# Performance work log

Hardware: AMD Instinct MI355X
Metric: run time of the kernel (lower is better)

The kernel has to match this reference:

```python
import jax, jax.numpy as jnp
import numpy as np

N, E, F_IN, HID, HEADS, B = 50000, 800000, 128, 128, 2, 256
EPS = 1e-5
NEG_SLOPE = 0.2


def gat_conv(x, src, dst, W, a_src, a_dst, b, heads, out_c, concat):
    n = x.shape[0]
    h = (x @ W).reshape(n, heads, out_c)            # [N,H,C]
    alpha_src = jnp.sum(h * a_src, axis=-1)          # [N,H]
    alpha_dst = jnp.sum(h * a_dst, axis=-1)          # [N,H]
    e = jax.nn.leaky_relu(alpha_src[src] + alpha_dst[dst], NEG_SLOPE)  # [E2,H]
    # segment softmax over incoming edges per destination node
    emax = jax.ops.segment_max(e, dst, num_segments=n)
    ex = jnp.exp(e - emax[dst])
    denom = jax.ops.segment_sum(ex, dst, num_segments=n)
    alpha = ex / denom[dst]                          # [E2,H]
    msg = h[src] * alpha[:, :, None]                 # [E2,H,C]
    out = jax.ops.segment_sum(msg, dst, num_segments=n)  # [N,H,C]
    if concat:
        out = out.reshape(n, heads * out_c)
    else:
        out = out.mean(axis=1)
    return out + b


def batchnorm_eval(x, gamma, beta, mean, var):
    return gamma * (x - mean) * jax.lax.rsqrt(var + EPS) + beta


def setup_inputs() -> dict:
    key = jax.random.key(0)
    ks = jax.random.split(key, 16)
    x = jax.random.normal(ks[0], (N, F_IN), dtype=jnp.float32)
    edge_index = jax.random.randint(ks[1], (2, E), 0, N, dtype=jnp.int64)
    batch = (jnp.arange(N, dtype=jnp.int64) * B) // N  # sorted, every graph non-empty
    s1 = 1.0 / np.sqrt(F_IN)
    s2 = 1.0 / np.sqrt(HEADS * HID)
    return {
        "x": x,
        "edge_index": edge_index,
        "batch": batch,
        "W1": jax.random.normal(ks[2], (F_IN, HEADS * HID), dtype=jnp.float32) * s1,
        "a_src1": jax.random.normal(ks[3], (HEADS, HID), dtype=jnp.float32) * s1,
        "a_dst1": jax.random.normal(ks[4], (HEADS, HID), dtype=jnp.float32) * s1,
        "b1": jnp.zeros((HEADS * HID,), dtype=jnp.float32),
        "gamma1": jnp.ones((HEADS * HID,), dtype=jnp.float32),
        "beta1": jnp.zeros((HEADS * HID,), dtype=jnp.float32),
        "rm1": jax.random.normal(ks[5], (HEADS * HID,), dtype=jnp.float32) * 0.1,
        "rv1": jax.random.uniform(ks[6], (HEADS * HID,), dtype=jnp.float32, minval=0.5, maxval=1.5),
        "W2": jax.random.normal(ks[7], (HEADS * HID, HID), dtype=jnp.float32) * s2,
        "a_src2": jax.random.normal(ks[8], (1, HID), dtype=jnp.float32) * s2,
        "a_dst2": jax.random.normal(ks[9], (1, HID), dtype=jnp.float32) * s2,
        "b2": jnp.zeros((HID,), dtype=jnp.float32),
        "gamma2": jnp.ones((HID,), dtype=jnp.float32),
        "beta2": jnp.zeros((HID,), dtype=jnp.float32),
        "rm2": jax.random.normal(ks[10], (HID,), dtype=jnp.float32) * 0.1,
        "rv2": jax.random.uniform(ks[11], (HID,), dtype=jnp.float32, minval=0.5, maxval=1.5),
    }


def reference(x, edge_index, batch, W1, a_src1, a_dst1, b1, gamma1, beta1, rm1, rv1,
              W2, a_src2, a_dst2, b2, gamma2, beta2, rm2, rv2):
    n = x.shape[0]
    # PyG GATConv adds self-loops by default
    loops = jnp.arange(n, dtype=edge_index.dtype)
    src = jnp.concatenate([edge_index[0], loops])
    dst = jnp.concatenate([edge_index[1], loops])

    h = gat_conv(x, src, dst, W1, a_src1, a_dst1, b1, HEADS, HID, concat=True)
    h = jax.nn.relu(batchnorm_eval(h, gamma1, beta1, rm1, rv1))  # dropout = identity (eval)

    h = gat_conv(h, src, dst, W2, a_src2, a_dst2, b2, 1, HID, concat=False)
    h = jax.nn.relu(batchnorm_eval(h, gamma2, beta2, rm2, rv2))

    # global max pool over graphs
    h_D = jax.ops.segment_max(h, batch, num_segments=B)  # [B, HID]
    return h_D
```

## Files before the change

### kernel.cpp

```cpp
#include <hip/hip_runtime.h>
#include <hip/hip_bf16.h>
#include <math.h>

#define NEG_SLOPE 0.2f
#define EPSBN 1e-5f

typedef __attribute__((ext_vector_type(8))) short bf16x8;
typedef __attribute__((ext_vector_type(4))) float f32x4;

__device__ __forceinline__ float bfu2f(unsigned u_lo16) { return __uint_as_float(u_lo16 << 16); }
__device__ __forceinline__ unsigned short f2bf(float f) {
    return __bfloat16_as_ushort(__float2bfloat16(f));
}
__device__ __forceinline__ void splitf(float v, unsigned short &h, unsigned short &l) {
    __hip_bfloat16 hb = __float2bfloat16(v);
    float r = v - __bfloat162float(hb);
    h = __bfloat16_as_ushort(hb);
    l = __bfloat16_as_ushort(__float2bfloat16(r));
}

__global__ void split_x4(const float* __restrict__ X, unsigned short* __restrict__ Xh,
                         unsigned short* __restrict__ Xl, int total4)
{
    int i = blockIdx.x * blockDim.x + threadIdx.x;
    if (i >= total4) return;
    float4 v = *(const float4*)(X + (size_t)i * 4);
    unsigned short h[4], l[4];
    splitf(v.x, h[0], l[0]); splitf(v.y, h[1], l[1]);
    splitf(v.z, h[2], l[2]); splitf(v.w, h[3], l[3]);
    *(uint2*)(Xh + (size_t)i * 4) = *(uint2*)h;
    *(uint2*)(Xl + (size_t)i * 4) = *(uint2*)l;
}

__global__ void split_w_both(const float* __restrict__ W1, const float* __restrict__ W2,
                             unsigned short* __restrict__ w1th, unsigned short* __restrict__ w1tl,
                             unsigned short* __restrict__ w2th, unsigned short* __restrict__ w2tl)
{
    int idx = blockIdx.x * blockDim.x + threadIdx.x;
    if (idx < 32768) {
        int nn = idx >> 7, k = idx & 127;
        unsigned short h, l; splitf(W1[(size_t)k * 256 + nn], h, l);
        w1th[idx] = h; w1tl[idx] = l;
    } else if (idx < 65536) {
        int j = idx - 32768;
        int nn = j >> 8, k = j & 255;
        unsigned short h, l; splitf(W2[(size_t)k * 128 + nn], h, l);
        w2th[j] = h; w2tl[j] = l;
    }
}

__global__ __launch_bounds__(256) void gemm_bf16_split_attn(
    const unsigned short* __restrict__ Ah, const unsigned short* __restrict__ Al,
    const unsigned short* __restrict__ Bth, const unsigned short* __restrict__ Btl,
    unsigned short* __restrict__ Cb,
    const float* __restrict__ aSrc, const float* __restrict__ aDst,
    float* __restrict__ asrcOut, float* __restrict__ adstOut,
    int M, int N, int K, int heads)
{
    __shared__ unsigned short smem[4][128][32];
    const int tid = threadIdx.x;
    const int lane = tid & 63;
    const int wave = tid >> 6;
    const int fr = lane & 15, g = lane >> 4;
    const int wr = (wave >> 1) * 64, wc = (wave & 1) * 64;
    const int rowBase = blockIdx.x * 128, colBase = blockIdx.y * 128;

    f32x4 acc[4][4] = {};

    for (int kk = 0; kk < K; kk += 32) {
#pragma unroll
        for (int i = 0; i < 2; ++i) {
            int idx = tid + 256 * i;
            int r = idx >> 2, c = (idx & 3) * 8;
            int grow = rowBase + r;
            uint4 va_h, va_l;
            if (grow < M) {
                va_h = *(const uint4*)(Ah + (size_t)grow * K + kk + c);
                va_l = *(const uint4*)(Al + (size_t)grow * K + kk + c);
            } else {
                va_h = make_uint4(0, 0, 0, 0); va_l = make_uint4(0, 0, 0, 0);
            }
            *(uint4*)&smem[0][r][c] = va_h;
            *(uint4*)&smem[1][r][c] = va_l;
            int gcol = colBase + r;
            *(uint4*)&smem[2][r][c] = *(const uint4*)(Bth + (size_t)gcol * K + kk + c);
            *(uint4*)&smem[3][r][c] = *(const uint4*)(Btl + (size_t)gcol * K + kk + c);
        }
        __syncthreads();

        bf16x8 ah[4], al[4], bh[4], bl[4];
#pragma unroll
        for (int m = 0; m < 4; ++m) {
            ah[m] = *(const bf16x8*)&smem[0][wr + m * 16 + fr][g * 8];
            al[m] = *(const bf16x8*)&smem[1][wr + m * 16 + fr][g * 8];
        }
#pragma unroll
        for (int n = 0; n < 4; ++n) {
            bh[n] = *(const bf16x8*)&smem[2][wc + n * 16 + fr][g * 8];
            bl[n] = *(const bf16x8*)&smem[3][wc + n * 16 + fr][g * 8];
        }
#pragma unroll
        for (int m = 0; m < 4; ++m)
#pragma unroll
            for (int n = 0; n < 4; ++n) {
                acc[m][n] = __builtin_amdgcn_mfma_f32_16x16x32_bf16(ah[m], bh[n], acc[m][n], 0, 0, 0);
                acc[m][n] = __builtin_amdgcn_mfma_f32_16x16x32_bf16(ah[m], bl[n], acc[m][n], 0, 0, 0);
                acc[m][n] = __builtin_amdgcn_mfma_f32_16x16x32_bf16(al[m], bh[n], acc[m][n], 0, 0, 0);
            }
        __syncthreads();
    }

    {
        const int head = colBase >> 7;
        float avs[4], avd[4];
#pragma unroll
        for (int n = 0; n < 4; ++n) {
            int col = colBase + wc + n * 16 + fr;
            avs[n] = aSrc[col]; avd[n] = aDst[col];
        }
#pragma unroll
        for (int m = 0; m < 4; ++m) {
            float ps[4], pd[4];
#pragma unroll
            for (int j = 0; j < 4; ++j) {
                ps[j] = acc[m][0][j] * avs[0] + acc[m][1][j] * avs[1]
                      + acc[m][2][j] * avs[2] + acc[m][3][j] * avs[3];
                pd[j] = acc[m][0][j] * avd[0] + acc[m][1][j] * avd[1]
                      + acc[m][2][j] * avd[2] + acc[m][3][j] * avd[3];
            }
#pragma unroll
            for (int off = 8; off; off >>= 1)
#pragma unroll
                for (int j = 0; j < 4; ++j) {
                    ps[j] += __shfl_xor(ps[j], off);
                    pd[j] += __shfl_xor(pd[j], off);
                }
            if (fr == 0) {
#pragma unroll
                for (int j = 0; j < 4; ++j) {
                    int grow = rowBase + wr + m * 16 + g * 4 + j;
                    if (grow < M) {
                        atomicAdd(asrcOut + (size_t)grow * heads + head, ps[j]);
                        atomicAdd(adstOut + (size_t)grow * heads + head, pd[j]);
                    }
                }
            }
        }
    }

    float* Cs = (float*)&smem[0][0][0];
    const int rl_w = (wr >> 6) * 16;
#pragma unroll
    for (int m = 0; m < 4; ++m) {
        __syncthreads();
#pragma unroll
        for (int n = 0; n < 4; ++n)
#pragma unroll
            for (int j = 0; j < 4; ++j)
                Cs[(rl_w + g * 4 + j) * 132 + wc + n * 16 + fr] = acc[m][n][j];
        __syncthreads();
        int rl = tid >> 3, c16 = (tid & 7) * 16;
        int grow = rowBase + (rl >> 4) * 64 + m * 16 + (rl & 15);
        if (grow < M) {
            unsigned short tmp[16];
#pragma unroll
            for (int i = 0; i < 16; ++i) tmp[i] = f2bf(Cs[rl * 132 + c16 + i]);
            *(uint4*)(Cb + (size_t)grow * N + colBase + c16)     = *(uint4*)&tmp[0];
            *(uint4*)(Cb + (size_t)grow * N + colBase + c16 + 8) = *(uint4*)&tmp[8];
        }
    }
}

__global__ void count_edges(const int* __restrict__ ei, int E, int Nn,
                            int* __restrict__ counts, int* __restrict__ erank)
{
    int e = blockIdx.x * blockDim.x + threadIdx.x;
    int E2 = E + Nn;
    if (e >= E2) return;
    int dst = (e < E) ? ei[E + e] : (e - E);
    erank[e] = atomicAdd(&counts[dst], 1);
}

__global__ __launch_bounds__(256) void scan_block(
    const int* __restrict__ counts, int* __restrict__ offs, int* __restrict__ bsum, int Nn)
{
    __shared__ int s[256];
    int i = blockIdx.x * 256 + threadIdx.x;
    int v = (i < Nn) ? counts[i] : 0;
    s[threadIdx.x] = v;
    __syncthreads();
    for (int off = 1; off < 256; off <<= 1) {
        int t = (threadIdx.x >= off) ? s[threadIdx.x - off] : 0;
        __syncthreads();
        s[threadIdx.x] += t;
        __syncthreads();
    }
    if (i < Nn) offs[i] = s[threadIdx.x] - v;
    if (threadIdx.x == 255) bsum[blockIdx.x] = s[255];
}

__global__ __launch_bounds__(256) void scan_tops(int* __restrict__ bsum, int* __restrict__ boff, int nb)
{
    __shared__ int s[256];
    int v = (threadIdx.x < nb) ? bsum[threadIdx.x] : 0;
    s[threadIdx.x] = v;
    __syncthreads();
    for (int off = 1; off < 256; off <<= 1) {
        int t = (threadIdx.x >= off) ? s[threadIdx.x - off] : 0;
        __syncthreads();
        s[threadIdx.x] += t;
        __syncthreads();
    }
    if (threadIdx.x < nb) boff[threadIdx.x] = s[threadIdx.x] - v;
}

__global__ void add_offsets(int* __restrict__ offs, const int* __restrict__ boff, int Nn, int E2)
{
    int i = blockIdx.x * blockDim.x + threadIdx.x;
    if (i < Nn) offs[i] += boff[i >> 8];
    if (i == 0) offs[Nn] = E2;
}

__global__ void fill_edges(const int* __restrict__ ei, int E, int Nn,
                           const int* __restrict__ offs, const int* __restrict__ erank,
                           int* __restrict__ esrc)
{
    int e = blockIdx.x * blockDim.x + threadIdx.x;
    int E2 = E + Nn;
    if (e >= E2) return;
    int src, dst;
    if (e < E) { src = ei[e]; dst = ei[E + e]; }
    else       { src = e - E; dst = e - E; }
    esrc[offs[dst] + erank[e]] = src;
}

__device__ __forceinline__ void fma8(float wA, uint4 hv, float acc[8])
{
    acc[0] = fmaf(wA, bfu2f(hv.x & 0xffff), acc[0]);
    acc[1] = fmaf(wA, __uint_as_float(hv.x & 0xffff0000u), acc[1]);
    acc[2] = fmaf(wA, bfu2f(hv.y & 0xffff), acc[2]);
    acc[3] = fmaf(wA, __uint_as_float(hv.y & 0xffff0000u), acc[3]);
    acc[4] = fmaf(wA, bfu2f(hv.z & 0xffff), acc[4]);
    acc[5] = fmaf(wA, __uint_as_float(hv.z & 0xffff0000u), acc[5]);
    acc[6] = fmaf(wA, bfu2f(hv.w & 0xffff), acc[6]);
    acc[7] = fmaf(wA, __uint_as_float(hv.w & 0xffff0000u), acc[7]);
}

__device__ __forceinline__ void gather2h(
    int sj, float w0, float w1, int nc, int sub, int head,
    const char* __restrict__ hb_c, float acc[8])
{
    int t = 0;
    for (; t + 8 <= nc; t += 8) {
        int e0 = t + sub;
        int sA0 = __shfl(sj, e0),     sA1 = __shfl(sj, e0 + 2);
        int sA2 = __shfl(sj, e0 + 4), sA3 = __shfl(sj, e0 + 6);
        float a0 = __shfl(w0, e0),     a1 = __shfl(w0, e0 + 2);
        float a2 = __shfl(w0, e0 + 4), a3 = __shfl(w0, e0 + 6);
        float b0 = __shfl(w1, e0),     b1 = __shfl(w1, e0 + 2);
        float b2 = __shfl(w1, e0 + 4), b3 = __shfl(w1, e0 + 6);
        uint4 h0 = *(const uint4*)(hb_c + sA0 * 512);
        uint4 h1 = *(const uint4*)(hb_c + sA1 * 512);
        uint4 h2 = *(const uint4*)(hb_c + sA2 * 512);
        uint4 h3 = *(const uint4*)(hb_c + sA3 * 512);
        fma8(head ? b0 : a0, h0, acc);
        fma8(head ? b1 : a1, h1, acc);
        fma8(head ? b2 : a2, h2, acc);
        fma8(head ? b3 : a3, h3, acc);
    }
    for (; t < nc; t += 2) {
        int e = t + sub;
        int sA = __shfl(sj, e);
        float a = __shfl(w0, e), b = __shfl(w1, e);
        uint4 hv = *(const uint4*)(hb_c + sA * 512);
        fma8(head ? b : a, hv, acc);
    }
}

__device__ __forceinline__ void gather1h(
    int sj, float w, int nc, int sub,
    const char* __restrict__ hb_c, float acc[8])
{
    int t = 0;
    for (; t + 16 <= nc; t += 16) {
        int e0 = t + sub;
        int sA0 = __shfl(sj, e0),     sA1 = __shfl(sj, e0 + 4);
        int sA2 = __shfl(sj, e0 + 8), sA3 = __shfl(sj, e0 + 12);
        float w0 = __shfl(w, e0),     w1 = __shfl(w, e0 + 4);
        float w2 = __shfl(w, e0 + 8), w3 = __shfl(w, e0 + 12);
        uint4 h0 = *(const uint4*)(hb_c + sA0 * 256);
        uint4 h1 = *(const uint4*)(hb_c + sA1 * 256);
        uint4 h2 = *(const uint4*)(hb_c + sA2 * 256);
        uint4 h3 = *(const uint4*)(hb_c + sA3 * 256);
        fma8(w0, h0, acc);
        fma8(w1, h1, acc);
        fma8(w2, h2, acc);
        fma8(w3, h3, acc);
    }
    for (; t < nc; t += 4) {
        int e = t + sub;
        int sA = __shfl(sj, e);
        float wA = __shfl(w, e);
        uint4 hv = *(const uint4*)(hb_c + sA * 256);
        fma8(wA, hv, acc);
    }
}

__global__ __launch_bounds__(256) void spmm1(
    const unsigned short* __restrict__ h1b, const float* __restrict__ asrc,
    const float* __restrict__ adst, const int* __restrict__ offs,
    const int* __restrict__ esrc,
    const float* __restrict__ b1, const float* __restrict__ gamma,
    const float* __restrict__ beta, const float* __restrict__ rm,
    const float* __restrict__ rv, unsigned short* __restrict__ x2h,
    unsigned short* __restrict__ x2l, int Nn)
{
    int d = (int)((blockIdx.x * blockDim.x + threadIdx.x) >> 6);
    int lane = threadIdx.x & 63;
    if (d >= Nn) return;
    int beg = offs[d], end = offs[d + 1];
    int deg = end - beg;
    float ad0 = adst[d * 2], ad1 = adst[d * 2 + 1];
    const int sub = lane >> 5;
    const int cgrp = lane & 31;
    const int head = cgrp >> 4;
    const char* hb_c = (const char*)h1b + cgrp * 16;
    float acc[8] = {};

    if (deg <= 64) {
        int sj = 0; float e0 = -1e30f, e1 = -1e30f;
        if (lane < deg) {
            sj = esrc[beg + lane];
            float2 av = *(const float2*)(asrc + (size_t)sj * 2);
            e0 = av.x + ad0; e0 = e0 > 0.f ? e0 : NEG_SLOPE * e0;
            e1 = av.y + ad1; e1 = e1 > 0.f ? e1 : NEG_SLOPE * e1;
        }
        float m0 = e0, m1 = e1;
        for (int off = 32; off; off >>= 1) {
            m0 = fmaxf(m0, __shfl_xor(m0, off));
            m1 = fmaxf(m1, __shfl_xor(m1, off));
        }
        float p0 = (lane < deg) ? expf(e0 - m0) : 0.f;
        float p1 = (lane < deg) ? expf(e1 - m1) : 0.f;
        float s0 = p0, s1 = p1;
        for (int off = 32; off; off >>= 1) {
            s0 += __shfl_xor(s0, off);
            s1 += __shfl_xor(s1, off);
        }
        float w0 = p0 * (1.f / s0), w1 = p1 * (1.f / s1);
        gather2h(sj, w0, w1, deg, sub, head, hb_c, acc);
    } else {
        float m0 = -1e30f, m1 = -1e30f;
        for (int j = beg + lane; j < end; j += 64) {
            int s = esrc[j];
            float2 av = *(const float2*)(asrc + (size_t)s * 2);
            float e0 = av.x + ad0; e0 = e0 > 0.f ? e0 : NEG_SLOPE * e0;
            float e1 = av.y + ad1; e1 = e1 > 0.f ? e1 : NEG_SLOPE * e1;
            m0 = fmaxf(m0, e0); m1 = fmaxf(m1, e1);
        }
        for (int off = 32; off; off >>= 1) {
            m0 = fmaxf(m0, __shfl_xor(m0, off));
            m1 = fmaxf(m1, __shfl_xor(m1, off));
        }
        float s0 = 0.f, s1 = 0.f;
        for (int j = beg + lane; j < end; j += 64) {
            int s = esrc[j];
            float2 av = *(const float2*)(asrc + (size_t)s * 2);
            float e0 = av.x + ad0; e0 = e0 > 0.f ? e0 : NEG_SLOPE * e0;
            float e1 = av.y + ad1; e1 = e1 > 0.f ? e1 : NEG_SLOPE * e1;
            s0 += expf(e0 - m0); s1 += expf(e1 - m1);
        }
        for (int off = 32; off; off >>= 1) {
            s0 += __shfl_xor(s0, off);
            s1 += __shfl_xor(s1, off);
        }
        float rd0 = 1.f / s0, rd1 = 1.f / s1;
        for (int base = beg; base < end; base += 64) {
            int nc = end - base; if (nc > 64) nc = 64;
            int sj = 0; float w0 = 0.f, w1 = 0.f;
            if (lane < nc) {
                sj = esrc[base + lane];
                float2 av = *(const float2*)(asrc + (size_t)sj * 2);
                float e0 = av.x + ad0; e0 = e0 > 0.f ? e0 : NEG_SLOPE * e0;
                float e1 = av.y + ad1; e1 = e1 > 0.f ? e1 : NEG_SLOPE * e1;
                w0 = expf(e0 - m0) * rd0;
                w1 = expf(e1 - m1) * rd1;
            }
            gather2h(sj, w0, w1, nc, sub, head, hb_c, acc);
        }
    }
#pragma unroll
    for (int i = 0; i < 8; ++i) acc[i] += __shfl_xor(acc[i], 32);
    if (lane < 32) {
        int cl = cgrp * 8;
        unsigned short hh[8], ll[8];
#pragma unroll
        for (int i = 0; i < 8; ++i) {
            int c = cl + i;
            float v = acc[i] + b1[c];
            v = gamma[c] * (v - rm[c]) * rsqrtf(rv[c] + EPSBN) + beta[c];
            v = fmaxf(v, 0.f);
            splitf(v, hh[i], ll[i]);
        }
        *(uint4*)(x2h + (size_t)d * 256 + cl) = *(uint4*)&hh[0];
        *(uint4*)(x2l + (size_t)d * 256 + cl) = *(uint4*)&ll[0];
    }
}

__global__ __launch_bounds__(256) void spmm2(
    const unsigned short* __restrict__ h2b, const float* __restrict__ asrc,
    const float* __restrict__ adst, const int* __restrict__ offs,
    const int* __restrict__ esrc,
    const float* __restrict__ b2, const float* __restrict__ gamma,
    const float* __restrict__ beta, const float* __restrict__ rm,
    const float* __restrict__ rv, float* __restrict__ x3, int Nn)
{
    int d = (int)((blockIdx.x * blockDim.x + threadIdx.x) >> 6);
    int lane = threadIdx.x & 63;
    if (d >= Nn) return;
    int beg = offs[d], end = offs[d + 1];
    int deg = end - beg;
    float ad = adst[d];
    const int sub = lane >> 4;
    const int cgrp = lane & 15;
    const char* hb_c = (const char*)h2b + cgrp * 16;
    float acc[8] = {};

    if (deg <= 64) {
        int sj = 0; float ev = -1e30f;
        if (lane < deg) {
            sj = esrc[beg + lane];
            float e = asrc[sj] + ad; ev = e > 0.f ? e : NEG_SLOPE * e;
        }
        float m = ev;
        for (int off = 32; off; off >>= 1) m = fmaxf(m, __shfl_xor(m, off));
        float p = (lane < deg) ? expf(ev - m) : 0.f;
        float s = p;
        for (int off = 32; off; off >>= 1) s += __shfl_xor(s, off);
        float w = p * (1.f / s);
        gather1h(sj, w, deg, sub, hb_c, acc);
    } else {
        float m = -1e30f;
        for (int j = beg + lane; j < end; j += 64) {
            int s = esrc[j];
            float e = asrc[s] + ad; e = e > 0.f ? e : NEG_SLOPE * e;
            m = fmaxf(m, e);
        }
        for (int off = 32; off; off >>= 1) m = fmaxf(m, __shfl_xor(m, off));
        float sd = 0.f;
        for (int j = beg + lane; j < end; j += 64) {
            int s = esrc[j];
            float e = asrc[s] + ad; e = e > 0.f ? e : NEG_SLOPE * e;
            sd += expf(e - m);
        }
        for (int off = 32; off; off >>= 1) sd += __shfl_xor(sd, off);
        float rd = 1.f / sd;
        for (int base = beg; base < end; base += 64) {
            int nc = end - base; if (nc > 64) nc = 64;
            int sj = 0; float wj = 0.f;
            if (lane < nc) {
                sj = esrc[base + lane];
                float e = asrc[sj] + ad; e = e > 0.f ? e : NEG_SLOPE * e;
                wj = expf(e - m) * rd;
            }
            gather1h(sj, wj, nc, sub, hb_c, acc);
        }
    }
#pragma unroll
    for (int i = 0; i < 8; ++i) {
        acc[i] += __shfl_xor(acc[i], 32);
        acc[i] += __shfl_xor(acc[i], 16);
    }
    if (lane < 16) {
        int cl = cgrp * 8;
        float vv[8];
#pragma unroll
        for (int i = 0; i < 8; ++i) {
            int c = cl + i;
            float v = acc[i] + b2[c];
            v = gamma[c] * (v - rm[c]) * rsqrtf(rv[c] + EPSBN) + beta[c];
            vv[i] = fmaxf(v, 0.f);
        }
        *(float4*)(x3 + (size_t)d * 128 + cl)     = make_float4(vv[0], vv[1], vv[2], vv[3]);
        *(float4*)(x3 + (size_t)d * 128 + cl + 4) = make_float4(vv[4], vv[5], vv[6], vv[7]);
    }
}

__global__ __launch_bounds__(128) void pool_max_graph(
    const float* __restrict__ x3, const int* __restrict__ bat,
    float* __restrict__ out, int Nn)
{
    int g = blockIdx.x;
    int c = threadIdx.x;
    int lo = 0, hi = Nn;
    while (lo < hi) { int mid = (lo + hi) >> 1; if (bat[mid] < g) lo = mid + 1; else hi = mid; }
    int beg = lo;
    hi = Nn;
    while (lo < hi) { int mid = (lo + hi) >> 1; if (bat[mid] < g + 1) lo = mid + 1; else hi = mid; }
    int end = lo;
    float acc = -1e30f;
    for (int n = beg; n < end; ++n)
        acc = fmaxf(acc, x3[(size_t)n * 128 + c]);
    out[(size_t)g * 128 + c] = acc;
}

extern "C" void kernel_launch(void* const* d_in, const int* in_sizes, int n_in,
                              void* d_out, int out_size, void* d_ws, size_t ws_size,
                              hipStream_t stream)
{
    const float* x   = (const float*)d_in[0];
    const int*   ei  = (const int*)d_in[1];
    const int*   bat = (const int*)d_in[2];
    const float* W1  = (const float*)d_in[3];
    const float* as1 = (const float*)d_in[4];
    const float* ad1 = (const float*)d_in[5];
    const float* b1  = (const float*)d_in[6];
    const float* g1  = (const float*)d_in[7];
    const float* be1 = (const float*)d_in[8];
    const float* rm1 = (const float*)d_in[9];
    const float* rv1 = (const float*)d_in[10];
    const float* W2  = (const float*)d_in[11];
    const float* as2 = (const float*)d_in[12];
    const float* ad2 = (const float*)d_in[13];
    const float* b2  = (const float*)d_in[14];
    const float* g2  = (const float*)d_in[15];
    const float* be2 = (const float*)d_in[16];
    const float* rm2 = (const float*)d_in[17];
    const float* rv2 = (const float*)d_in[18];
    float* out = (float*)d_out;

    const int Nn = in_sizes[0] / 128;
    const int E  = in_sizes[1] / 2;
    const int E2 = E + Nn;
    const int B  = out_size / 128;

    char* p = (char*)d_ws;
    size_t off = 0;
    auto alloc = [&](size_t bytes) -> void* {
        void* r = p + off;
        off = (off + bytes + 255) & ~(size_t)255;
        return r;
    };
    unsigned short* xh    = (unsigned short*)alloc((size_t)Nn * 128 * 2);
    unsigned short* xl    = (unsigned short*)alloc((size_t)Nn * 128 * 2);
    unsigned short* w1th  = (unsigned short*)alloc(256 * 128 * 2);
    unsigned short* w1tl  = (unsigned short*)alloc(256 * 128 * 2);
    unsigned short* w2th  = (unsigned short*)alloc(128 * 256 * 2);
    unsigned short* w2tl  = (unsigned short*)alloc(128 * 256 * 2);
    unsigned short* h1b   = (unsigned short*)alloc((size_t)Nn * 256 * 2);
    unsigned short* x2h   = (unsigned short*)alloc((size_t)Nn * 256 * 2);
    unsigned short* x2l   = (unsigned short*)alloc((size_t)Nn * 256 * 2);
    unsigned short* h2b   = (unsigned short*)alloc((size_t)Nn * 128 * 2);
    float*          x3    = (float*)alloc((size_t)Nn * 128 * 4);
    float*          attnv = (float*)alloc((size_t)Nn * 6 * 4);
    float*          asrc1 = attnv;
    float*          adst1 = attnv + (size_t)Nn * 2;
    float*          asrc2 = attnv + (size_t)Nn * 4;
    float*          adst2 = attnv + (size_t)Nn * 5;
    int*            counts= (int*)alloc((size_t)Nn * 4);
    int*            erank = (int*)alloc((size_t)E2 * 4);
    int*            offs  = (int*)alloc((size_t)(Nn + 1) * 4);
    int*            bsum  = (int*)alloc(256 * 4);
    int*            boff  = (int*)alloc(256 * 4);
    int*            esrc  = (int*)alloc((size_t)E2 * 4);

    const int nb = (Nn + 255) / 256;
    const int nwB = (Nn + 3) / 4;
    const int gmB = (Nn + 127) / 128;

    hipMemsetAsync(counts, 0, (size_t)Nn * 4, stream);
    hipMemsetAsync(attnv, 0, (size_t)Nn * 6 * 4, stream);

    split_x4<<<(Nn * 128 / 4 + 255) / 256, 256, 0, stream>>>(x, xh, xl, Nn * 128 / 4);
    split_w_both<<<(65536 + 255) / 256, 256, 0, stream>>>(W1, W2, w1th, w1tl, w2th, w2tl);

    count_edges<<<(E2 + 255) / 256, 256, 0, stream>>>(ei, E, Nn, counts, erank);
    scan_block<<<nb, 256, 0, stream>>>(counts, offs, bsum, Nn);
    scan_tops<<<1, 256, 0, stream>>>(bsum, boff, nb);
    add_offsets<<<(Nn + 255) / 256, 256, 0, stream>>>(offs, boff, Nn, E2);
    fill_edges<<<(E2 + 255) / 256, 256, 0, stream>>>(ei, E, Nn, offs, erank, esrc);

    gemm_bf16_split_attn<<<dim3(gmB, 2), 256, 0, stream>>>(
        xh, xl, w1th, w1tl, h1b, as1, ad1, asrc1, adst1, Nn, 256, 128, 2);
    spmm1<<<nwB, 256, 0, stream>>>(h1b, asrc1, adst1, offs, esrc,
                                   b1, g1, be1, rm1, rv1, x2h, x2l, Nn);

    gemm_bf16_split_attn<<<dim3(gmB, 1), 256, 0, stream>>>(
        x2h, x2l, w2th, w2tl, h2b, as2, ad2, asrc2, adst2, Nn, 128, 256, 1);
    spmm2<<<nwB, 256, 0, stream>>>(h2b, asrc2, adst2, offs, esrc,
                                   b2, g2, be2, rm2, rv2, x3, Nn);

    pool_max_graph<<<B, 128, 0, stream>>>(x3, bat, out, Nn);
}
```

Baseline: 281.3 us.

## Reorder layer-1 GAT to aggregate raw features before the weight GEMM

Layer-1 attention logits are now computed directly from x using precomputed vectors W1·a_src and W1·a_dst, fused into the input split kernel. The sparse aggregation then gathers 128-wide raw input rows (256 B bf16) per edge instead of 256-wide projected rows, producing a per-head aggregated input [N,256]. A new GEMM applies each head's W1 slice and fuses bias, batchnorm and ReLU into its epilogue. This halves the gather traffic per edge in exchange for writing and re-reading a larger split-precision intermediate. Layer-1 aggregation also loses precision, since it now sums bf16-rounded x (high part only) where the old path summed bf16 h.

```diff
diff --git a/kernel.cpp b/kernel.cpp
--- a/kernel.cpp
+++ b/kernel.cpp
@@ -19,17 +19,48 @@
     l = __bfloat16_as_ushort(__float2bfloat16(r));
 }
 
-__global__ void split_x4(const float* __restrict__ X, unsigned short* __restrict__ Xh,
-                         unsigned short* __restrict__ Xl, int total4)
-{
-    int i = blockIdx.x * blockDim.x + threadIdx.x;
-    if (i >= total4) return;
-    float4 v = *(const float4*)(X + (size_t)i * 4);
-    unsigned short h[4], l[4];
-    splitf(v.x, h[0], l[0]); splitf(v.y, h[1], l[1]);
-    splitf(v.z, h[2], l[2]); splitf(v.w, h[3], l[3]);
-    *(uint2*)(Xh + (size_t)i * 4) = *(uint2*)h;
-    *(uint2*)(Xl + (size_t)i * 4) = *(uint2*)l;
+__global__ void precompute_v(const float* __restrict__ W1, const float* __restrict__ as1,
+                             const float* __restrict__ ad1, float* __restrict__ vsd)
+{
+    int k = threadIdx.x;
+    if (k >= 128) return;
+    float v0 = 0.f, v1 = 0.f, v2 = 0.f, v3 = 0.f;
+    const float* wr = W1 + (size_t)k * 256;
+    for (int c = 0; c < 128; ++c) {
+        float wa = wr[c], wb = wr[128 + c];
+        v0 += wa * as1[c];  v1 += wb * as1[128 + c];
+        v2 += wa * ad1[c];  v3 += wb * ad1[128 + c];
+    }
+    vsd[k] = v0; vsd[128 + k] = v1; vsd[256 + k] = v2; vsd[384 + k] = v3;
+}
+
+__global__ __launch_bounds__(256) void split_x_attn(
+    const float* __restrict__ X, const float* __restrict__ vsd,
+    unsigned short* __restrict__ Xh, unsigned short* __restrict__ Xl,
+    float* __restrict__ asrc, float* __restrict__ adst, int Nn)
+{
+    int n = (int)((blockIdx.x * blockDim.x + threadIdx.x) >> 6);
+    int lane = threadIdx.x & 63;
+    if (n >= Nn) return;
+    float2 xv = *(const float2*)(X + (size_t)n * 128 + lane * 2);
+    unsigned short h0, l0, h1, l1;
+    splitf(xv.x, h0, l0); splitf(xv.y, h1, l1);
+    unsigned short hh[2] = {h0, h1}, ll[2] = {l0, l1};
+    *(unsigned*)(Xh + (size_t)n * 128 + lane * 2) = *(unsigned*)hh;
+    *(unsigned*)(Xl + (size_t)n * 128 + lane * 2) = *(unsigned*)ll;
+    int k = lane * 2;
+    float p0 = xv.x * vsd[k]       + xv.y * vsd[k + 1];
+    float p1 = xv.x * vsd[128 + k] + xv.y * vsd[129 + k];
+    float p2 = xv.x * vsd[256 + k] + xv.y * vsd[257 + k];
+    float p3 = xv.x * vsd[384 + k] + xv.y * vsd[385 + k];
+    for (int off = 32; off; off >>= 1) {
+        p0 += __shfl_xor(p0, off); p1 += __shfl_xor(p1, off);
+        p2 += __shfl_xor(p2, off); p3 += __shfl_xor(p3, off);
+    }
+    if (lane == 0) {
+        asrc[n * 2] = p0; asrc[n * 2 + 1] = p1;
+        adst[n * 2] = p2; adst[n * 2 + 1] = p3;
+    }
 }
 
 __global__ void split_w_both(const float* __restrict__ W1, const float* __restrict__ W2,
@@ -46,6 +77,329 @@
         int nn = j >> 8, k = j & 255;
         unsigned short h, l; splitf(W2[(size_t)k * 128 + nn], h, l);
         w2th[j] = h; w2tl[j] = l;
+    }
+}
+
+__global__ void count_edges(const int* __restrict__ ei, int E, int Nn,
+                            int* __restrict__ counts, int* __restrict__ erank)
+{
+    int e = blockIdx.x * blockDim.x + threadIdx.x;
+    int E2 = E + Nn;
+    if (e >= E2) return;
+    int dst = (e < E) ? ei[E + e] : (e - E);
+    erank[e] = atomicAdd(&counts[dst], 1);
+}
+
+__global__ __launch_bounds__(256) void scan_block(
+    const int* __restrict__ counts, int* __restrict__ offs, int* __restrict__ bsum, int Nn)
+{
+    __shared__ int s[256];
+    int i = blockIdx.x * 256 + threadIdx.x;
+    int v = (i < Nn) ? counts[i] : 0;
+    s[threadIdx.x] = v;
+    __syncthreads();
+    for (int off = 1; off < 256; off <<= 1) {
+        int t = (threadIdx.x >= off) ? s[threadIdx.x - off] : 0;
+        __syncthreads();
+        s[threadIdx.x] += t;
+        __syncthreads();
+    }
+    if (i < Nn) offs[i] = s[threadIdx.x] - v;
+    if (threadIdx.x == 255) bsum[blockIdx.x] = s[255];
+}
+
+__global__ __launch_bounds__(256) void scan_tops(int* __restrict__ bsum, int* __restrict__ boff, int nb)
+{
+    __shared__ int s[256];
+    int v = (threadIdx.x < nb) ? bsum[threadIdx.x] : 0;
+    s[threadIdx.x] = v;
+    __syncthreads();
+    for (int off = 1; off < 256; off <<= 1) {
+        int t = (threadIdx.x >= off) ? s[threadIdx.x - off] : 0;
+        __syncthreads();
+        s[threadIdx.x] += t;
+        __syncthreads();
+    }
+    if (threadIdx.x < nb) boff[threadIdx.x] = s[threadIdx.x] - v;
+}
+
+__global__ void add_offsets(int* __restrict__ offs, const int* __restrict__ boff, int Nn, int E2)
+{
+    int i = blockIdx.x * blockDim.x + threadIdx.x;
+    if (i < Nn) offs[i] += boff[i >> 8];
+    if (i == 0) offs[Nn] = E2;
+}
+
+__global__ void fill_edges(const int* __restrict__ ei, int E, int Nn,
+                           const int* __restrict__ offs, const int* __restrict__ erank,
+                           int* __restrict__ esrc)
+{
+    int e = blockIdx.x * blockDim.x + threadIdx.x;
+    int E2 = E + Nn;
+    if (e >= E2) return;
+    int src, dst;
+    if (e < E) { src = ei[e]; dst = ei[E + e]; }
+    else       { src = e - E; dst = e - E; }
+    esrc[offs[dst] + erank[e]] = src;
+}
+
+__device__ __forceinline__ void fma8(float wA, uint4 hv, float acc[8])
+{
+    acc[0] = fmaf(wA, bfu2f(hv.x & 0xffff), acc[0]);
+    acc[1] = fmaf(wA, __uint_as_float(hv.x & 0xffff0000u), acc[1]);
+    acc[2] = fmaf(wA, bfu2f(hv.y & 0xffff), acc[2]);
+    acc[3] = fmaf(wA, __uint_as_float(hv.y & 0xffff0000u), acc[3]);
+    acc[4] = fmaf(wA, bfu2f(hv.z & 0xffff), acc[4]);
+    acc[5] = fmaf(wA, __uint_as_float(hv.z & 0xffff0000u), acc[5]);
+    acc[6] = fmaf(wA, bfu2f(hv.w & 0xffff), acc[6]);
+    acc[7] = fmaf(wA, __uint_as_float(hv.w & 0xffff0000u), acc[7]);
+}
+
+__device__ __forceinline__ void fma8x2(float wa, float wb, uint4 hv,
+                                       float a0[8], float a1[8])
+{
+    float f;
+    f = bfu2f(hv.x & 0xffff);                 a0[0]=fmaf(wa,f,a0[0]); a1[0]=fmaf(wb,f,a1[0]);
+    f = __uint_as_float(hv.x & 0xffff0000u);  a0[1]=fmaf(wa,f,a0[1]); a1[1]=fmaf(wb,f,a1[1]);
+    f = bfu2f(hv.y & 0xffff);                 a0[2]=fmaf(wa,f,a0[2]); a1[2]=fmaf(wb,f,a1[2]);
+    f = __uint_as_float(hv.y & 0xffff0000u);  a0[3]=fmaf(wa,f,a0[3]); a1[3]=fmaf(wb,f,a1[3]);
+    f = bfu2f(hv.z & 0xffff);                 a0[4]=fmaf(wa,f,a0[4]); a1[4]=fmaf(wb,f,a1[4]);
+    f = __uint_as_float(hv.z & 0xffff0000u);  a0[5]=fmaf(wa,f,a0[5]); a1[5]=fmaf(wb,f,a1[5]);
+    f = bfu2f(hv.w & 0xffff);                 a0[6]=fmaf(wa,f,a0[6]); a1[6]=fmaf(wb,f,a1[6]);
+    f = __uint_as_float(hv.w & 0xffff0000u);  a0[7]=fmaf(wa,f,a0[7]); a1[7]=fmaf(wb,f,a1[7]);
+}
+
+__device__ __forceinline__ void gather1h(
+    int sj, float w, int nc, int sub,
+    const char* __restrict__ hb_c, float acc[8])
+{
+    for (int t = 0; t < nc; t += 4) {
+        int e = t + sub;
+        int sA = __shfl(sj, e);
+        float wA = __shfl(w, e);
+        uint4 hv = *(const uint4*)(hb_c + sA * 256);
+        fma8(wA, hv, acc);
+    }
+}
+
+__device__ __forceinline__ void gatherx(
+    int sj, float w0, float w1, int nc, int sub,
+    const char* __restrict__ hb_c, float a0[8], float a1[8])
+{
+    for (int t = 0; t < nc; t += 4) {
+        int e = t + sub;
+        int sA = __shfl(sj, e);
+        float wa = __shfl(w0, e);
+        float wb = __shfl(w1, e);
+        uint4 hv = *(const uint4*)(hb_c + sA * 256);
+        fma8x2(wa, wb, hv, a0, a1);
+    }
+}
+
+__global__ __launch_bounds__(256) void spmm_x(
+    const unsigned short* __restrict__ xh, const float* __restrict__ asrc,
+    const float* __restrict__ adst, const int* __restrict__ offs,
+    const int* __restrict__ esrc,
+    unsigned short* __restrict__ xth, unsigned short* __restrict__ xtl, int Nn)
+{
+    int d = (int)((blockIdx.x * blockDim.x + threadIdx.x) >> 6);
+    int lane = threadIdx.x & 63;
+    if (d >= Nn) return;
+    int beg = offs[d], end = offs[d + 1];
+    int deg = end - beg;
+    float ad0 = adst[d * 2], ad1 = adst[d * 2 + 1];
+    const int sub = lane >> 4;
+    const int cgrp = lane & 15;
+    const char* hb_c = (const char*)xh + cgrp * 16;
+    float a0[8] = {}, a1[8] = {};
+
+    if (deg <= 64) {
+        int sj = 0; float e0 = -1e30f, e1 = -1e30f;
+        if (lane < deg) {
+            sj = esrc[beg + lane];
+            float2 av = *(const float2*)(asrc + (size_t)sj * 2);
+            e0 = av.x + ad0; e0 = e0 > 0.f ? e0 : NEG_SLOPE * e0;
+            e1 = av.y + ad1; e1 = e1 > 0.f ? e1 : NEG_SLOPE * e1;
+        }
+        float m0 = e0, m1 = e1;
+        for (int off = 32; off; off >>= 1) {
+            m0 = fmaxf(m0, __shfl_xor(m0, off));
+            m1 = fmaxf(m1, __shfl_xor(m1, off));
+        }
+        float p0 = (lane < deg) ? expf(e0 - m0) : 0.f;
+        float p1 = (lane < deg) ? expf(e1 - m1) : 0.f;
+        float s0 = p0, s1 = p1;
+        for (int off = 32; off; off >>= 1) {
+            s0 += __shfl_xor(s0, off);
+            s1 += __shfl_xor(s1, off);
+        }
+        float w0 = p0 * (1.f / s0), w1 = p1 * (1.f / s1);
+        gatherx(sj, w0, w1, deg, sub, hb_c, a0, a1);
+    } else {
+        float m0 = -1e30f, m1 = -1e30f;
+        for (int j = beg + lane; j < end; j += 64) {
+            int s = esrc[j];
+            float2 av = *(const float2*)(asrc + (size_t)s * 2);
+            float e0 = av.x + ad0; e0 = e0 > 0.f ? e0 : NEG_SLOPE * e0;
+            float e1 = av.y + ad1; e1 = e1 > 0.f ? e1 : NEG_SLOPE * e1;
+            m0 = fmaxf(m0, e0); m1 = fmaxf(m1, e1);
+        }
+        for (int off = 32; off; off >>= 1) {
+            m0 = fmaxf(m0, __shfl_xor(m0, off));
+            m1 = fmaxf(m1, __shfl_xor(m1, off));
+        }
+        float s0 = 0.f, s1 = 0.f;
+        for (int j = beg + lane; j < end; j += 64) {
+            int s = esrc[j];
+            float2 av = *(const float2*)(asrc + (size_t)s * 2);
+            float e0 = av.x + ad0; e0 = e0 > 0.f ? e0 : NEG_SLOPE * e0;
+            float e1 = av.y + ad1; e1 = e1 > 0.f ? e1 : NEG_SLOPE * e1;
+            s0 += expf(e0 - m0); s1 += expf(e1 - m1);
+        }
+        for (int off = 32; off; off >>= 1) {
+            s0 += __shfl_xor(s0, off);
+            s1 += __shfl_xor(s1, off);
+        }
+        float rd0 = 1.f / s0, rd1 = 1.f / s1;
+        for (int base = beg; base < end; base += 64) {
+            int nc = end - base; if (nc > 64) nc = 64;
+            int sj = 0; float w0 = 0.f, w1 = 0.f;
+            if (lane < nc) {
+                sj = esrc[base + lane];
+                float2 av = *(const float2*)(asrc + (size_t)sj * 2);
+                float e0 = av.x + ad0; e0 = e0 > 0.f ? e0 : NEG_SLOPE * e0;
+                float e1 = av.y + ad1; e1 = e1 > 0.f ? e1 : NEG_SLOPE * e1;
+                w0 = expf(e0 - m0) * rd0;
+                w1 = expf(e1 - m1) * rd1;
+            }
+            gatherx(sj, w0, w1, nc, sub, hb_c, a0, a1);
+        }
+    }
+#pragma unroll
+    for (int i = 0; i < 8; ++i) {
+        a0[i] += __shfl_xor(a0[i], 32); a0[i] += __shfl_xor(a0[i], 16);
+        a1[i] += __shfl_xor(a1[i], 32); a1[i] += __shfl_xor(a1[i], 16);
+    }
+    if (lane < 16) {
+        int cl = cgrp * 8;
+        unsigned short h0[8], l0[8], h1[8], l1[8];
+#pragma unroll
+        for (int i = 0; i < 8; ++i) {
+            splitf(a0[i], h0[i], l0[i]);
+            splitf(a1[i], h1[i], l1[i]);
+        }
+        size_t rb = (size_t)d * 256;
+        *(uint4*)(xth + rb + cl)       = *(uint4*)&h0[0];
+        *(uint4*)(xtl + rb + cl)       = *(uint4*)&l0[0];
+        *(uint4*)(xth + rb + 128 + cl) = *(uint4*)&h1[0];
+        *(uint4*)(xtl + rb + 128 + cl) = *(uint4*)&l1[0];
+    }
+}
+
+__global__ __launch_bounds__(256) void gemm_bn_split(
+    const unsigned short* __restrict__ Ah, const unsigned short* __restrict__ Al,
+    const unsigned short* __restrict__ Bth, const unsigned short* __restrict__ Btl,
+    const float* __restrict__ bias, const float* __restrict__ gamma,
+    const float* __restrict__ beta, const float* __restrict__ rm,
+    const float* __restrict__ rv,
+    unsigned short* __restrict__ Ch, unsigned short* __restrict__ Cl, int M)
+{
+    __shared__ unsigned short smem[4][128][32];
+    const int tid = threadIdx.x;
+    const int lane = tid & 63;
+    const int wave = tid >> 6;
+    const int fr = lane & 15, g = lane >> 4;
+    const int wr = (wave >> 1) * 64, wc = (wave & 1) * 64;
+    const int rowBase = blockIdx.x * 128, colBase = blockIdx.y * 128;
+
+    f32x4 acc[4][4] = {};
+
+    for (int kk = 0; kk < 128; kk += 32) {
+#pragma unroll
+        for (int i = 0; i < 2; ++i) {
+            int idx = tid + 256 * i;
+            int r = idx >> 2, c = (idx & 3) * 8;
+            int grow = rowBase + r;
+            uint4 va_h, va_l;
+            if (grow < M) {
+                va_h = *(const uint4*)(Ah + (size_t)grow * 256 + colBase + kk + c);
+                va_l = *(const uint4*)(Al + (size_t)grow * 256 + colBase + kk + c);
+            } else {
+                va_h = make_uint4(0, 0, 0, 0); va_l = make_uint4(0, 0, 0, 0);
+            }
+            *(uint4*)&smem[0][r][c] = va_h;
+            *(uint4*)&smem[1][r][c] = va_l;
+            int gcol = colBase + r;
+            *(uint4*)&smem[2][r][c] = *(const uint4*)(Bth + (size_t)gcol * 128 + kk + c);
+            *(uint4*)&smem[3][r][c] = *(const uint4*)(Btl + (size_t)gcol * 128 + kk + c);
+        }
+        __syncthreads();
+
+        bf16x8 ah[4], al[4], bh[4], bl[4];
+#pragma unroll
+        for (int m = 0; m < 4; ++m) {
+            ah[m] = *(const bf16x8*)&smem[0][wr + m * 16 + fr][g * 8];
+            al[m] = *(const bf16x8*)&smem[1][wr + m * 16 + fr][g * 8];
+        }
+#pragma unroll
+        for (int n = 0; n < 4; ++n) {
+            bh[n] = *(const bf16x8*)&smem[2][wc + n * 16 + fr][g * 8];
+            bl[n] = *(const bf16x8*)&smem[3][wc + n * 16 + fr][g * 8];
+        }
+#pragma unroll
+        for (int m = 0; m < 4; ++m)
+#pragma unroll
+            for (int n = 0; n < 4; ++n) {
+                acc[m][n] = __builtin_amdgcn_mfma_f32_16x16x32_bf16(ah[m], bh[n], acc[m][n], 0, 0, 0);
+                acc[m][n] = __builtin_amdgcn_mfma_f32_16x16x32_bf16(ah[m], bl[n], acc[m][n], 0, 0, 0);
+                acc[m][n] = __builtin_amdgcn_mfma_f32_16x16x32_bf16(al[m], bh[n], acc[m][n], 0, 0, 0);
+            }
+        __syncthreads();
+    }
+
+    {
+        float bi[4], ga[4], bb[4], mu[4], iv[4];
+#pragma unroll
+        for (int n = 0; n < 4; ++n) {
+            int c = colBase + wc + n * 16 + fr;
+            bi[n] = bias[c]; ga[n] = gamma[c]; bb[n] = beta[c];
+            mu[n] = rm[c];   iv[n] = rsqrtf(rv[c] + EPSBN);
+        }
+#pragma unroll
+        for (int m = 0; m < 4; ++m)
+#pragma unroll
+            for (int n = 0; n < 4; ++n)
+#pragma unroll
+                for (int j = 0; j < 4; ++j) {
+                    float v = acc[m][n][j] + bi[n];
+                    v = ga[n] * (v - mu[n]) * iv[n] + bb[n];
+                    acc[m][n][j] = fmaxf(v, 0.f);
+                }
+    }
+
+    float* Cs = (float*)&smem[0][0][0];
+    const int rl_w = (wr >> 6) * 16;
+#pragma unroll
+    for (int m = 0; m < 4; ++m) {
+        __syncthreads();
+#pragma unroll
+        for (int n = 0; n < 4; ++n)
+#pragma unroll
+            for (int j = 0; j < 4; ++j)
+                Cs[(rl_w + g * 4 + j) * 132 + wc + n * 16 + fr] = acc[m][n][j];
+        __syncthreads();
+        int rl = tid >> 3, c16 = (tid & 7) * 16;
+        int grow = rowBase + (rl >> 4) * 64 + m * 16 + (rl & 15);
+        if (grow < M) {
+            unsigned short th[16], tl[16];
+#pragma unroll
+            for (int i = 0; i < 16; ++i) splitf(Cs[rl * 132 + c16 + i], th[i], tl[i]);
+            size_t ob = (size_t)grow * 256 + colBase + c16;
+            *(uint4*)(Ch + ob)     = *(uint4*)&th[0];
+            *(uint4*)(Ch + ob + 8) = *(uint4*)&th[8];
+            *(uint4*)(Cl + ob)     = *(uint4*)&tl[0];
+            *(uint4*)(Cl + ob + 8) = *(uint4*)&tl[8];
+        }
     }
 }
 
@@ -168,242 +522,6 @@
             *(uint4*)(Cb + (size_t)grow * N + colBase + c16)     = *(uint4*)&tmp[0];
             *(uint4*)(Cb + (size_t)grow * N + colBase + c16 + 8) = *(uint4*)&tmp[8];
         }
-    }
-}
-
-__global__ void count_edges(const int* __restrict__ ei, int E, int Nn,
-                            int* __restrict__ counts, int* __restrict__ erank)
-{
-    int e = blockIdx.x * blockDim.x + threadIdx.x;
-    int E2 = E + Nn;
-    if (e >= E2) return;
-    int dst = (e < E) ? ei[E + e] : (e - E);
-    erank[e] = atomicAdd(&counts[dst], 1);
-}
-
-__global__ __launch_bounds__(256) void scan_block(
-    const int* __restrict__ counts, int* __restrict__ offs, int* __restrict__ bsum, int Nn)
-{
-    __shared__ int s[256];
-    int i = blockIdx.x * 256 + threadIdx.x;
-    int v = (i < Nn) ? counts[i] : 0;
-    s[threadIdx.x] = v;
-    __syncthreads();
-    for (int off = 1; off < 256; off <<= 1) {
-        int t = (threadIdx.x >= off) ? s[threadIdx.x - off] : 0;
-        __syncthreads();
-        s[threadIdx.x] += t;
-        __syncthreads();
-    }
-    if (i < Nn) offs[i] = s[threadIdx.x] - v;
-    if (threadIdx.x == 255) bsum[blockIdx.x] = s[255];
-}
-
-__global__ __launch_bounds__(256) void scan_tops(int* __restrict__ bsum, int* __restrict__ boff, int nb)
-{
-    __shared__ int s[256];
-    int v = (threadIdx.x < nb) ? bsum[threadIdx.x] : 0;
-    s[threadIdx.x] = v;
-    __syncthreads();
-    for (int off = 1; off < 256; off <<= 1) {
-        int t = (threadIdx.x >= off) ? s[threadIdx.x - off] : 0;
-        __syncthreads();
-        s[threadIdx.x] += t;
-        __syncthreads();
-    }
-    if (threadIdx.x < nb) boff[threadIdx.x] = s[threadIdx.x] - v;
-}
-
-__global__ void add_offsets(int* __restrict__ offs, const int* __restrict__ boff, int Nn, int E2)
-{
-    int i = blockIdx.x * blockDim.x + threadIdx.x;
-    if (i < Nn) offs[i] += boff[i >> 8];
-    if (i == 0) offs[Nn] = E2;
-}
-
-__global__ void fill_edges(const int* __restrict__ ei, int E, int Nn,
-                           const int* __restrict__ offs, const int* __restrict__ erank,
-                           int* __restrict__ esrc)
-{
-    int e = blockIdx.x * blockDim.x + threadIdx.x;
-    int E2 = E + Nn;
-    if (e >= E2) return;
-    int src, dst;
-    if (e < E) { src = ei[e]; dst = ei[E + e]; }
-    else       { src = e - E; dst = e - E; }
-    esrc[offs[dst] + erank[e]] = src;
-}
-
-__device__ __forceinline__ void fma8(float wA, uint4 hv, float acc[8])
-{
-    acc[0] = fmaf(wA, bfu2f(hv.x & 0xffff), acc[0]);
-    acc[1] = fmaf(wA, __uint_as_float(hv.x & 0xffff0000u), acc[1]);
-    acc[2] = fmaf(wA, bfu2f(hv.y & 0xffff), acc[2]);
-    acc[3] = fmaf(wA, __uint_as_float(hv.y & 0xffff0000u), acc[3]);
-    acc[4] = fmaf(wA, bfu2f(hv.z & 0xffff), acc[4]);
-    acc[5] = fmaf(wA, __uint_as_float(hv.z & 0xffff0000u), acc[5]);
-    acc[6] = fmaf(wA, bfu2f(hv.w & 0xffff), acc[6]);
-    acc[7] = fmaf(wA, __uint_as_float(hv.w & 0xffff0000u), acc[7]);
-}
-
-__device__ __forceinline__ void gather2h(
-    int sj, float w0, float w1, int nc, int sub, int head,
-    const char* __restrict__ hb_c, float acc[8])
-{
-    int t = 0;
-    for (; t + 8 <= nc; t += 8) {
-        int e0 = t + sub;
-        int sA0 = __shfl(sj, e0),     sA1 = __shfl(sj, e0 + 2);
-        int sA2 = __shfl(sj, e0 + 4), sA3 = __shfl(sj, e0 + 6);
-        float a0 = __shfl(w0, e0),     a1 = __shfl(w0, e0 + 2);
-        float a2 = __shfl(w0, e0 + 4), a3 = __shfl(w0, e0 + 6);
-        float b0 = __shfl(w1, e0),     b1 = __shfl(w1, e0 + 2);
-        float b2 = __shfl(w1, e0 + 4), b3 = __shfl(w1, e0 + 6);
-        uint4 h0 = *(const uint4*)(hb_c + sA0 * 512);
-        uint4 h1 = *(const uint4*)(hb_c + sA1 * 512);
-        uint4 h2 = *(const uint4*)(hb_c + sA2 * 512);
-        uint4 h3 = *(const uint4*)(hb_c + sA3 * 512);
-        fma8(head ? b0 : a0, h0, acc);
-        fma8(head ? b1 : a1, h1, acc);
-        fma8(head ? b2 : a2, h2, acc);
-        fma8(head ? b3 : a3, h3, acc);
-    }
-    for (; t < nc; t += 2) {
-        int e = t + sub;
-        int sA = __shfl(sj, e);
-        float a = __shfl(w0, e), b = __shfl(w1, e);
-        uint4 hv = *(const uint4*)(hb_c + sA * 512);
-        fma8(head ? b : a, hv, acc);
-    }
-}
-
-__device__ __forceinline__ void gather1h(
-    int sj, float w, int nc, int sub,
-    const char* __restrict__ hb_c, float acc[8])
-{
-    int t = 0;
-    for (; t + 16 <= nc; t += 16) {
-        int e0 = t + sub;
-        int sA0 = __shfl(sj, e0),     sA1 = __shfl(sj, e0 + 4);
-        int sA2 = __shfl(sj, e0 + 8), sA3 = __shfl(sj, e0 + 12);
-        float w0 = __shfl(w, e0),     w1 = __shfl(w, e0 + 4);
-        float w2 = __shfl(w, e0 + 8), w3 = __shfl(w, e0 + 12);
-        uint4 h0 = *(const uint4*)(hb_c + sA0 * 256);
-        uint4 h1 = *(const uint4*)(hb_c + sA1 * 256);
-        uint4 h2 = *(const uint4*)(hb_c + sA2 * 256);
-        uint4 h3 = *(const uint4*)(hb_c + sA3 * 256);
-        fma8(w0, h0, acc);
-        fma8(w1, h1, acc);
-        fma8(w2, h2, acc);
-        fma8(w3, h3, acc);
-    }
-    for (; t < nc; t += 4) {
-        int e = t + sub;
-        int sA = __shfl(sj, e);
-        float wA = __shfl(w, e);
-        uint4 hv = *(const uint4*)(hb_c + sA * 256);
-        fma8(wA, hv, acc);
-    }
-}
-
-__global__ __launch_bounds__(256) void spmm1(
-    const unsigned short* __restrict__ h1b, const float* __restrict__ asrc,
-    const float* __restrict__ adst, const int* __restrict__ offs,
-    const int* __restrict__ esrc,
-    const float* __restrict__ b1, const float* __restrict__ gamma,
-    const float* __restrict__ beta, const float* __restrict__ rm,
-    const float* __restrict__ rv, unsigned short* __restrict__ x2h,
-    unsigned short* __restrict__ x2l, int Nn)
-{
-    int d = (int)((blockIdx.x * blockDim.x + threadIdx.x) >> 6);
-    int lane = threadIdx.x & 63;
-    if (d >= Nn) return;
-    int beg = offs[d], end = offs[d + 1];
-    int deg = end - beg;
-    float ad0 = adst[d * 2], ad1 = adst[d * 2 + 1];
-    const int sub = lane >> 5;
-    const int cgrp = lane & 31;
-    const int head = cgrp >> 4;
-    const char* hb_c = (const char*)h1b + cgrp * 16;
-    float acc[8] = {};
-
-    if (deg <= 64) {
-        int sj = 0; float e0 = -1e30f, e1 = -1e30f;
-        if (lane < deg) {
-            sj = esrc[beg + lane];
-            float2 av = *(const float2*)(asrc + (size_t)sj * 2);
-            e0 = av.x + ad0; e0 = e0 > 0.f ? e0 : NEG_SLOPE * e0;
-            e1 = av.y + ad1; e1 = e1 > 0.f ? e1 : NEG_SLOPE * e1;
-        }
-        float m0 = e0, m1 = e1;
-        for (int off = 32; off; off >>= 1) {
-            m0 = fmaxf(m0, __shfl_xor(m0, off));
-            m1 = fmaxf(m1, __shfl_xor(m1, off));
-        }
-        float p0 = (lane < deg) ? expf(e0 - m0) : 0.f;
-        float p1 = (lane < deg) ? expf(e1 - m1) : 0.f;
-        float s0 = p0, s1 = p1;
-        for (int off = 32; off; off >>= 1) {
-            s0 += __shfl_xor(s0, off);
-            s1 += __shfl_xor(s1, off);
-        }
-        float w0 = p0 * (1.f / s0), w1 = p1 * (1.f / s1);
-        gather2h(sj, w0, w1, deg, sub, head, hb_c, acc);
-    } else {
-        float m0 = -1e30f, m1 = -1e30f;
-        for (int j = beg + lane; j < end; j += 64) {
-            int s = esrc[j];
-            float2 av = *(const float2*)(asrc + (size_t)s * 2);
-            float e0 = av.x + ad0; e0 = e0 > 0.f ? e0 : NEG_SLOPE * e0;
-            float e1 = av.y + ad1; e1 = e1 > 0.f ? e1 : NEG_SLOPE * e1;
-            m0 = fmaxf(m0, e0); m1 = fmaxf(m1, e1);
-        }
-        for (int off = 32; off; off >>= 1) {
-            m0 = fmaxf(m0, __shfl_xor(m0, off));
-            m1 = fmaxf(m1, __shfl_xor(m1, off));
-        }
-        float s0 = 0.f, s1 = 0.f;
-        for (int j = beg + lane; j < end; j += 64) {
-            int s = esrc[j];
-            float2 av = *(const float2*)(asrc + (size_t)s * 2);
-            float e0 = av.x + ad0; e0 = e0 > 0.f ? e0 : NEG_SLOPE * e0;
-            float e1 = av.y + ad1; e1 = e1 > 0.f ? e1 : NEG_SLOPE * e1;
-            s0 += expf(e0 - m0); s1 += expf(e1 - m1);
-        }
-        for (int off = 32; off; off >>= 1) {
-            s0 += __shfl_xor(s0, off);
-            s1 += __shfl_xor(s1, off);
-        }
-        float rd0 = 1.f / s0, rd1 = 1.f / s1;
-        for (int base = beg; base < end; base += 64) {
-            int nc = end - base; if (nc > 64) nc = 64;
-            int sj = 0; float w0 = 0.f, w1 = 0.f;
-            if (lane < nc) {
-                sj = esrc[base + lane];
-                float2 av = *(const float2*)(asrc + (size_t)sj * 2);
-                float e0 = av.x + ad0; e0 = e0 > 0.f ? e0 : NEG_SLOPE * e0;
-                float e1 = av.y + ad1; e1 = e1 > 0.f ? e1 : NEG_SLOPE * e1;
-                w0 = expf(e0 - m0) * rd0;
-                w1 = expf(e1 - m1) * rd1;
-            }
-            gather2h(sj, w0, w1, nc, sub, head, hb_c, acc);
-        }
-    }
-#pragma unroll
-    for (int i = 0; i < 8; ++i) acc[i] += __shfl_xor(acc[i], 32);
-    if (lane < 32) {
-        int cl = cgrp * 8;
-        unsigned short hh[8], ll[8];
-#pragma unroll
-        for (int i = 0; i < 8; ++i) {
-            int c = cl + i;
-            float v = acc[i] + b1[c];
-            v = gamma[c] * (v - rm[c]) * rsqrtf(rv[c] + EPSBN) + beta[c];
-            v = fmaxf(v, 0.f);
-            splitf(v, hh[i], ll[i]);
-        }
-        *(uint4*)(x2h + (size_t)d * 256 + cl) = *(uint4*)&hh[0];
-        *(uint4*)(x2l + (size_t)d * 256 + cl) = *(uint4*)&ll[0];
     }
 }
 
@@ -547,31 +665,34 @@
     unsigned short* w1tl  = (unsigned short*)alloc(256 * 128 * 2);
     unsigned short* w2th  = (unsigned short*)alloc(128 * 256 * 2);
     unsigned short* w2tl  = (unsigned short*)alloc(128 * 256 * 2);
-    unsigned short* h1b   = (unsigned short*)alloc((size_t)Nn * 256 * 2);
+    unsigned short* xth   = (unsigned short*)alloc((size_t)Nn * 256 * 2);
+    unsigned short* xtl   = (unsigned short*)alloc((size_t)Nn * 256 * 2);
     unsigned short* x2h   = (unsigned short*)alloc((size_t)Nn * 256 * 2);
     unsigned short* x2l   = (unsigned short*)alloc((size_t)Nn * 256 * 2);
-    unsigned short* h2b   = (unsigned short*)alloc((size_t)Nn * 128 * 2);
-    float*          x3    = (float*)alloc((size_t)Nn * 128 * 4);
-    float*          attnv = (float*)alloc((size_t)Nn * 6 * 4);
-    float*          asrc1 = attnv;
-    float*          adst1 = attnv + (size_t)Nn * 2;
-    float*          asrc2 = attnv + (size_t)Nn * 4;
-    float*          adst2 = attnv + (size_t)Nn * 5;
+    float*          vsd   = (float*)alloc(4 * 128 * 4);
+    float*          asrc1 = (float*)alloc((size_t)Nn * 2 * 4);
+    float*          adst1 = (float*)alloc((size_t)Nn * 2 * 4);
+    float*          attnv = (float*)alloc((size_t)Nn * 2 * 4);
+    float*          asrc2 = attnv;
+    float*          adst2 = attnv + Nn;
     int*            counts= (int*)alloc((size_t)Nn * 4);
     int*            erank = (int*)alloc((size_t)E2 * 4);
     int*            offs  = (int*)alloc((size_t)(Nn + 1) * 4);
     int*            bsum  = (int*)alloc(256 * 4);
     int*            boff  = (int*)alloc(256 * 4);
     int*            esrc  = (int*)alloc((size_t)E2 * 4);
+    float*          x3    = (float*)xth;
+    unsigned short* h2b   = xh;
 
     const int nb = (Nn + 255) / 256;
     const int nwB = (Nn + 3) / 4;
     const int gmB = (Nn + 127) / 128;
 
     hipMemsetAsync(counts, 0, (size_t)Nn * 4, stream);
-    hipMemsetAsync(attnv, 0, (size_t)Nn * 6 * 4, stream);
-
-    split_x4<<<(Nn * 128 / 4 + 255) / 256, 256, 0, stream>>>(x, xh, xl, Nn * 128 / 4);
+    hipMemsetAsync(attnv, 0, (size_t)Nn * 2 * 4, stream);
+
+    precompute_v<<<1, 128, 0, stream>>>(W1, as1, ad1, vsd);
+    split_x_attn<<<nwB, 256, 0, stream>>>(x, vsd, xh, xl, asrc1, adst1, Nn);
     split_w_both<<<(65536 + 255) / 256, 256, 0, stream>>>(W1, W2, w1th, w1tl, w2th, w2tl);
 
     count_edges<<<(E2 + 255) / 256, 256, 0, stream>>>(ei, E, Nn, counts, erank);
@@ -580,10 +701,9 @@
     add_offsets<<<(Nn + 255) / 256, 256, 0, stream>>>(offs, boff, Nn, E2);
     fill_edges<<<(E2 + 255) / 256, 256, 0, stream>>>(ei, E, Nn, offs, erank, esrc);
 
-    gemm_bf16_split_attn<<<dim3(gmB, 2), 256, 0, stream>>>(
-        xh, xl, w1th, w1tl, h1b, as1, ad1, asrc1, adst1, Nn, 256, 128, 2);
-    spmm1<<<nwB, 256, 0, stream>>>(h1b, asrc1, adst1, offs, esrc,
-                                   b1, g1, be1, rm1, rv1, x2h, x2l, Nn);
+    spmm_x<<<nwB, 256, 0, stream>>>(xh, asrc1, adst1, offs, esrc, xth, xtl, Nn);
+    gemm_bn_split<<<dim3(gmB, 2), 256, 0, stream>>>(
+        xth, xtl, w1th, w1tl, b1, g1, be1, rm1, rv1, x2h, x2l, Nn);
 
     gemm_bf16_split_attn<<<dim3(gmB, 1), 256, 0, stream>>>(
         x2h, x2l, w2th, w2tl, h2b, as2, ad2, asrc2, adst2, Nn, 128, 256, 1);
```

Result: faster. 272.8 us (-3.0%).
